# Kernel optimization log

Hardware: AMD Instinct MI355X
Metric: run time of the kernel (lower is better)

The kernel has to match this reference:

```python
import jax, jax.numpy as jnp
import numpy as np

B, N, G = 256, 512, 117  # batch, max_num_cells, n_genes
CH = 25                  # Emphsis conv out channels (hidden_d_1st_conv)


def setup_inputs() -> dict:
    key = jax.random.key(0)
    ks = jax.random.split(key, 11)
    images = jax.random.normal(ks[0], (B, N, 1, 7, 7), dtype=jnp.float32)
    spot_images = jax.random.normal(ks[1], (B, 1, 28, 28), dtype=jnp.float32)
    gene_expression = jax.random.normal(ks[2], (B, G), dtype=jnp.float32)
    # Emphsis: Conv2d(1, 25, k=3, s=1) + ReLU
    W_emph = jax.random.normal(ks[3], (CH, 1, 3, 3), dtype=jnp.float32) * 0.2
    b_emph = jax.random.normal(ks[4], (CH,), dtype=jnp.float32) * 0.1
    # 117 stacked GeneBlock Linear(625, 1) heads -> one (G, 625) matrix
    W_reg = jax.random.normal(ks[5], (G, 625), dtype=jnp.float32) * 0.04
    b_reg = jax.random.normal(ks[6], (G,), dtype=jnp.float32) * 0.1
    # PatchEmbedding: Conv2d(1, 3, k=5, s=5)
    W_patch = jax.random.normal(ks[7], (3, 1, 5, 5), dtype=jnp.float32) * 0.2
    b_patch = jax.random.normal(ks[8], (3,), dtype=jnp.float32) * 0.1
    # global_embedding: Linear(75, 1) + ELU
    W_glob = jax.random.normal(ks[9], (1, 75), dtype=jnp.float32) * 0.1
    b_glob = jax.random.normal(ks[10], (1,), dtype=jnp.float32) * 0.1
    return dict(images=images, spot_images=spot_images, gene_expression=gene_expression,
                W_emph=W_emph, b_emph=b_emph, W_reg=W_reg, b_reg=b_reg,
                W_patch=W_patch, b_patch=b_patch, W_glob=W_glob, b_glob=b_glob)


def reference(images, spot_images, gene_expression, W_emph, b_emph, W_reg, b_reg,
              W_patch, b_patch, W_glob, b_glob):
    Bn, Nc = images.shape[0], images.shape[1]
    # Emphsis conv over all (batch, cell) pairs at once: (B*N, 1, 7, 7) -> (B*N, 25, 5, 5)
    x = images.reshape(Bn * Nc, 1, 7, 7)
    t = jax.lax.conv_general_dilated(x, W_emph, window_strides=(1, 1), padding='VALID',
                                     dimension_numbers=('NCHW', 'OIHW', 'NCHW'))
    t = jax.nn.relu(t + b_emph[None, :, None, None])
    flat = t.reshape(Bn, Nc, CH * 5 * 5)  # (B, N, 625)
    # 117 independent Linear(625,1) heads fused into one matmul -> (B, N, G)
    out = jnp.einsum('bnd,gd->bng', flat, W_reg) + b_reg
    # PatchEmbedding: (B,1,28,28) -> (B,3,5,5) -> tokens (B,25,3) -> flatten (B,75)
    s = jax.lax.conv_general_dilated(spot_images, W_patch, window_strides=(5, 5), padding='VALID',
                                     dimension_numbers=('NCHW', 'OIHW', 'NCHW'))
    s = s + b_patch[None, :, None, None]
    s = s.reshape(Bn, 3, 25).transpose(0, 2, 1).reshape(Bn, 75)
    glob = jax.nn.elu(s @ W_glob.T + b_glob)  # (B, 1)
    # out1 broadcast of global embedding over (cells, genes)
    cell = jax.nn.relu(out + glob[:, :, None])  # (B, N, G)
    # F.linear with ones weight over cell axis == sum over cells
    spot = cell.sum(axis=1)  # (B, G)
    out1 = jnp.broadcast_to(glob[:, :, None], (Bn, Nc, out.shape[2]))  # (B, N, G)
    return spot, cell, out1
```

## Files before the change

### kernel.cpp

```cpp
#include <hip/hip_runtime.h>


typedef __attribute__((ext_vector_type(16))) float f32x16;
typedef __attribute__((ext_vector_type(8))) short short8;
typedef __attribute__((ext_vector_type(2))) unsigned int uint2v;
typedef __attribute__((ext_vector_type(4))) unsigned int uint4v;

#define WB_OFF    0
#define WBIG_OFF  163840
#define GLOB_OFF  245760
#define SPOT_OFF  246784

#define SPOT_OUT_OFF 0
#define CELL_OUT_OFF 29952
#define OUT1_OUT_OFF 15365376

__device__ __forceinline__ unsigned short f2bf(float x) {
  unsigned int u = __builtin_bit_cast(unsigned int, x);
  u = (u + 0x7FFFu + ((u >> 16) & 1u)) >> 16;
  return (unsigned short)u;
}

__device__ __forceinline__ unsigned int cvt_pk_bf16(float lo, float hi) {
  unsigned int w;
  asm("v_cvt_pk_bf16_f32 %0, %1, %2" : "=v"(w) : "v"(lo), "v"(hi));
  return w;
}

__global__ __launch_bounds__(128) void prep_kernel(
    const float* __restrict__ spot_images, const float* __restrict__ W_patch,
    const float* __restrict__ b_patch, const float* __restrict__ W_glob,
    const float* __restrict__ b_glob, const float* __restrict__ W_reg,
    const float* __restrict__ W_emph, const float* __restrict__ b_emph,
    unsigned short* __restrict__ wb, unsigned short* __restrict__ wbig,
    float* __restrict__ glob) {
  int bid = blockIdx.x;
  int tid = threadIdx.x;
  if (bid < 256) {
    __shared__ float red[75];
    if (tid < 75) {
      int token = tid / 3;
      int chan = tid - token * 3;
      int ty = token / 5, tx = token - ty * 5;
      const float* img = spot_images + bid * 784 + (ty * 5) * 28 + tx * 5;
      float a = 0.f;
      #pragma unroll
      for (int i = 0; i < 5; ++i)
        #pragma unroll
        for (int j = 0; j < 5; ++j)
          a = fmaf(img[i * 28 + j], W_patch[chan * 25 + i * 5 + j], a);
      a += b_patch[chan];
      red[tid] = a * W_glob[tid];
    }
    __syncthreads();
    if (tid == 0) {
      float s = b_glob[0];
      for (int k = 0; k < 75; ++k) s += red[k];
      glob[bid] = (s > 0.f) ? s : expm1f(s);
    }
  } else if (bid < 336) {
    int idx = bid - 256;
    int jt = idx >> 2, s = idx & 3;
    if (tid < 64) {
      int j = jt * 32 + (tid & 31);
      int h = tid >> 5;
      unsigned short hv[8];
      #pragma unroll
      for (int jj = 0; jj < 8; ++jj) {
        int i = s * 16 + h * 8 + jj;
        float val = 0.f;
        if (j < 625) {
          int ch = j / 25, p = j % 25;
          int oy = p / 5, ox = p - oy * 5;
          if (i < 49) {
            int iy = i / 7, ix = i - iy * 7;
            int ky = iy - oy, kx = ix - ox;
            if (ky >= 0 && ky < 3 && kx >= 0 && kx < 3)
              val = W_emph[ch * 9 + ky * 3 + kx];
          } else if (i == 49) {
            val = b_emph[ch];
          }
        }
        hv[jj] = f2bf(val);
      }
      unsigned int u[4];
      #pragma unroll
      for (int k = 0; k < 4; ++k)
        u[k] = (unsigned int)hv[2 * k] | ((unsigned int)hv[2 * k + 1] << 16);
      ((uint4*)wbig)[idx * 64 + tid] = make_uint4(u[0], u[1], u[2], u[3]);
    }
  } else {
    int idx = bid - 336;
    int sg = idx >> 2, wcp = idx & 3;
    if (tid < 64) {
      int g = wcp * 32 + (tid & 31);
      int h = tid >> 5;
      unsigned short hv[8];
      #pragma unroll
      for (int jj = 0; jj < 8; ++jj) {
        int k = sg * 16 + h * 8 + jj;
        float val = (g < 117 && k < 625) ? W_reg[g * 625 + k] : 0.f;
        hv[jj] = f2bf(val);
      }
      unsigned int u[4];
      #pragma unroll
      for (int k = 0; k < 4; ++k)
        u[k] = (unsigned int)hv[2 * k] | ((unsigned int)hv[2 * k + 1] << 16);
      ((uint4*)wb)[idx * 64 + tid] = make_uint4(u[0], u[1], u[2], u[3]);
    }
  }
}

__global__ __launch_bounds__(512, 4) void main_kernel(
    const float* __restrict__ images, const float* __restrict__ b_reg,
    const unsigned short* __restrict__ wb, const unsigned short* __restrict__ wbig,
    const float* __restrict__ glob, float* __restrict__ out,
    float* __restrict__ spotp) {
  __shared__ char smem[34816];
  unsigned short* imgbs = (unsigned short*)smem;
  float* C = (float*)smem;
  float* red = (float*)(smem + 32768);
  int tid = threadIdx.x;
  int bid = blockIdx.x;
  int b = bid >> 1, half = bid & 1;
  int n0 = half * 256;

  #pragma unroll
  for (int it = 0; it < 4; ++it) {
    int u = it * 512 + tid;
    int cell = u & 255, kc = u >> 8;
    const float* src = images + (size_t)(b * 512 + n0 + cell) * 49 + kc * 8;
    float v[8];
    #pragma unroll
    for (int j = 0; j < 8; ++j) v[j] = 0.f;
    if (kc < 6) {
      #pragma unroll
      for (int j = 0; j < 8; ++j) v[j] = src[j];
    } else if (kc == 6) {
      v[0] = src[0];
      v[1] = 1.0f;
    }
    unsigned int uu[4];
    #pragma unroll
    for (int k = 0; k < 4; ++k) uu[k] = cvt_pk_bf16(v[2 * k], v[2 * k + 1]);
    ((uint4*)imgbs)[kc * 256 + cell] = make_uint4(uu[0], uu[1], uu[2], uu[3]);
  }
  __syncthreads();

  int l = tid & 63;
  int ct = __builtin_amdgcn_readfirstlane(tid >> 6);
  int m = l & 31, hh = l >> 5;
  const short8* imgb8 = (const short8*)imgbs;
  const short8* wb8 = (const short8*)wb;
  const short8* wbig8 = (const short8*)wbig;

  short8 bi0 = imgb8[(0 + hh) * 256 + ct * 32 + m];
  short8 bi1 = imgb8[(2 + hh) * 256 + ct * 32 + m];
  short8 bi2 = imgb8[(4 + hh) * 256 + ct * 32 + m];
  short8 bi3 = imgb8[(6 + hh) * 256 + ct * 32 + m];

  f32x16 acc0, acc1, acc2, acc3;
  #pragma unroll
  for (int i = 0; i < 16; ++i) {
    acc0[i] = 0.f; acc1[i] = 0.f; acc2[i] = 0.f; acc3[i] = 0.f;
  }

  for (int jt = 0; jt < 20; ++jt) {
    int ab = jt * 256 + l;
    short8 a0 = wbig8[ab];
    short8 a1 = wbig8[ab + 64];
    short8 a2 = wbig8[ab + 128];
    short8 a3 = wbig8[ab + 192];

    f32x16 o;
    #pragma unroll
    for (int i = 0; i < 16; ++i) o[i] = 0.f;
    o = __builtin_amdgcn_mfma_f32_32x32x16_bf16(a0, bi0, o, 0, 0, 0);
    o = __builtin_amdgcn_mfma_f32_32x32x16_bf16(a1, bi1, o, 0, 0, 0);
    o = __builtin_amdgcn_mfma_f32_32x32x16_bf16(a2, bi2, o, 0, 0, 0);
    o = __builtin_amdgcn_mfma_f32_32x32x16_bf16(a3, bi3, o, 0, 0, 0);

    unsigned int W[8];
    #pragma unroll
    for (int q = 0; q < 8; ++q)
      W[q] = cvt_pk_bf16(fmaxf(o[2 * q], 0.f), fmaxf(o[2 * q + 1], 0.f));
    uint2v s02 = __builtin_amdgcn_permlane32_swap(W[0], W[2], false, false);
    uint2v s13 = __builtin_amdgcn_permlane32_swap(W[1], W[3], false, false);
    uint2v s46 = __builtin_amdgcn_permlane32_swap(W[4], W[6], false, false);
    uint2v s57 = __builtin_amdgcn_permlane32_swap(W[5], W[7], false, false);
    uint4v f0 = {s02[0], s13[0], s02[1], s13[1]};
    uint4v f1 = {s46[0], s57[0], s46[1], s57[1]};
    short8 af0 = __builtin_bit_cast(short8, f0);
    short8 af1 = __builtin_bit_cast(short8, f1);

    int kb = jt * 512 + l;
    acc0 = __builtin_amdgcn_mfma_f32_32x32x16_bf16(af0, wb8[kb], acc0, 0, 0, 0);
    acc1 = __builtin_amdgcn_mfma_f32_32x32x16_bf16(af0, wb8[kb + 64], acc1, 0, 0, 0);
    acc2 = __builtin_amdgcn_mfma_f32_32x32x16_bf16(af0, wb8[kb + 128], acc2, 0, 0, 0);
    acc3 = __builtin_amdgcn_mfma_f32_32x32x16_bf16(af0, wb8[kb + 192], acc3, 0, 0, 0);
    acc0 = __builtin_amdgcn_mfma_f32_32x32x16_bf16(af1, wb8[kb + 256], acc0, 0, 0, 0);
    acc1 = __builtin_amdgcn_mfma_f32_32x32x16_bf16(af1, wb8[kb + 320], acc1, 0, 0, 0);
    acc2 = __builtin_amdgcn_mfma_f32_32x32x16_bf16(af1, wb8[kb + 384], acc2, 0, 0, 0);
    acc3 = __builtin_amdgcn_mfma_f32_32x32x16_bf16(af1, wb8[kb + 448], acc3, 0, 0, 0);
  }
  __syncthreads();

  float gb = glob[b];
  float part = 0.f;
  size_t rowbase = (size_t)(b * 512 + n0);
  #pragma unroll
  for (int p = 0; p < 4; ++p) {
    if ((ct >> 1) == p) {
      int nb = (ct & 1) * 32;
      #define EPI(Q, ACC)                                                  \
        {                                                                  \
          int g = (Q)*32 + m;                                              \
          float br = (g < 117) ? b_reg[g] : 0.f;                           \
          _Pragma("unroll")                                                \
          for (int reg = 0; reg < 16; ++reg) {                             \
            int n = nb + (reg & 3) + 8 * (reg >> 2) + 4 * hh;              \
            C[n * 128 + g] = fmaxf(ACC[reg] + br + gb, 0.f);               \
          }                                                                \
        }
      EPI(0, acc0) EPI(1, acc1) EPI(2, acc2) EPI(3, acc3)
      #undef EPI
    }
    __syncthreads();
    float* cellchunk = out + CELL_OUT_OFF + (rowbase + p * 64) * 117;
    #pragma unroll
    for (int i = 0; i < 15; ++i) {
      int idx = i * 512 + tid;
      if (idx < 7488) {
        int n = idx / 117;
        int gg = idx - n * 117;
        cellchunk[idx] = C[n * 128 + gg];
      }
    }
    float4 gv = make_float4(gb, gb, gb, gb);
    float4* o1v = (float4*)(out + OUT1_OUT_OFF + (rowbase + p * 64) * 117);
    #pragma unroll
    for (int i = 0; i < 4; ++i) {
      int idx = i * 512 + tid;
      if (idx < 1872) o1v[idx] = gv;
    }
    {
      int grp = tid >> 7, t = tid & 127;
      float s = 0.f;
      #pragma unroll
      for (int n = 0; n < 16; ++n) s += C[(grp * 16 + n) * 128 + t];
      red[grp * 128 + t] = s;
    }
    __syncthreads();
    if (tid < 128)
      part += red[tid] + red[128 + tid] + red[256 + tid] + red[384 + tid];
  }
  if (tid < 128)
    spotp[(size_t)(b * 2 + half) * 128 + tid] = part;
}

__global__ __launch_bounds__(256) void spot_reduce(
    const float* __restrict__ spotp, float* __restrict__ out) {
  int idx = blockIdx.x * 256 + threadIdx.x;
  int b = idx / 117;
  int g = idx - b * 117;
  float s = spotp[(size_t)(b * 2 + 0) * 128 + g] +
            spotp[(size_t)(b * 2 + 1) * 128 + g];
  out[SPOT_OUT_OFF + idx] = s;
}

extern "C" void kernel_launch(void* const* d_in, const int* in_sizes, int n_in,
                              void* d_out, int out_size, void* d_ws, size_t ws_size,
                              hipStream_t stream) {
  const float* images      = (const float*)d_in[0];
  const float* spot_images = (const float*)d_in[1];
  const float* W_emph = (const float*)d_in[3];
  const float* b_emph = (const float*)d_in[4];
  const float* W_reg  = (const float*)d_in[5];
  const float* b_reg  = (const float*)d_in[6];
  const float* W_patch = (const float*)d_in[7];
  const float* b_patch = (const float*)d_in[8];
  const float* W_glob  = (const float*)d_in[9];
  const float* b_glob  = (const float*)d_in[10];
  float* out = (float*)d_out;

  unsigned short* wb   = (unsigned short*)((char*)d_ws + WB_OFF);
  unsigned short* wbig = (unsigned short*)((char*)d_ws + WBIG_OFF);
  float* glob  = (float*)((char*)d_ws + GLOB_OFF);
  float* spotp = (float*)((char*)d_ws + SPOT_OFF);

  prep_kernel<<<496, 128, 0, stream>>>(spot_images, W_patch, b_patch, W_glob,
                                       b_glob, W_reg, W_emph, b_emph, wb, wbig,
                                       glob);
  main_kernel<<<512, 512, 0, stream>>>(images, b_reg, wb, wbig, glob, out,
                                       spotp);
  spot_reduce<<<117, 256, 0, stream>>>(spotp, out);
}
```

Before: 61.87 us.

## Double-buffer combined weight tiles into LDS via async global_load_lds

Weights for both GEMM stages are interleaved per k-tile into one buffer. Each iteration asynchronously stages the next 12 KB tile into LDS with global_load_lds while computing on the current tile, replacing direct per-wave global loads. Because every wave read the same weights, they are now fetched once per block and shared, with the load latency meant to overlap compute. In exchange, LDS use per block rises to about 58 KB, which may limit occupancy, and a __syncthreads is added every iteration.

Measured after the change: 55.73 us. 1.11x faster.

```diff
diff --git a/kernel.cpp b/kernel.cpp
--- a/kernel.cpp
+++ b/kernel.cpp
@@ -6,8 +6,7 @@
 typedef __attribute__((ext_vector_type(2))) unsigned int uint2v;
 typedef __attribute__((ext_vector_type(4))) unsigned int uint4v;
 
-#define WB_OFF    0
-#define WBIG_OFF  163840
+#define WCOMB_OFF 0
 #define GLOB_OFF  245760
 #define SPOT_OFF  246784
 
@@ -25,6 +24,12 @@
   unsigned int w;
   asm("v_cvt_pk_bf16_f32 %0, %1, %2" : "=v"(w) : "v"(lo), "v"(hi));
   return w;
+}
+
+__device__ __forceinline__ void gload16(const void* g, void* l) {
+  __builtin_amdgcn_global_load_lds(
+      (const __attribute__((address_space(1))) void*)g,
+      (__attribute__((address_space(3))) void*)l, 16, 0, 0);
 }
 
 __global__ __launch_bounds__(128) void prep_kernel(
@@ -32,8 +37,7 @@
     const float* __restrict__ b_patch, const float* __restrict__ W_glob,
     const float* __restrict__ b_glob, const float* __restrict__ W_reg,
     const float* __restrict__ W_emph, const float* __restrict__ b_emph,
-    unsigned short* __restrict__ wb, unsigned short* __restrict__ wbig,
-    float* __restrict__ glob) {
+    unsigned short* __restrict__ wcomb, float* __restrict__ glob) {
   int bid = blockIdx.x;
   int tid = threadIdx.x;
   if (bid < 256) {
@@ -87,13 +91,13 @@
       #pragma unroll
       for (int k = 0; k < 4; ++k)
         u[k] = (unsigned int)hv[2 * k] | ((unsigned int)hv[2 * k + 1] << 16);
-      ((uint4*)wbig)[idx * 64 + tid] = make_uint4(u[0], u[1], u[2], u[3]);
+      ((uint4*)wcomb)[jt * 768 + s * 64 + tid] = make_uint4(u[0], u[1], u[2], u[3]);
     }
   } else {
     int idx = bid - 336;
-    int sg = idx >> 2, wcp = idx & 3;
+    int sg = idx >> 2, q = idx & 3;
     if (tid < 64) {
-      int g = wcp * 32 + (tid & 31);
+      int g = q * 32 + (tid & 31);
       int h = tid >> 5;
       unsigned short hv[8];
       #pragma unroll
@@ -106,24 +110,37 @@
       #pragma unroll
       for (int k = 0; k < 4; ++k)
         u[k] = (unsigned int)hv[2 * k] | ((unsigned int)hv[2 * k + 1] << 16);
-      ((uint4*)wb)[idx * 64 + tid] = make_uint4(u[0], u[1], u[2], u[3]);
+      int jt = sg >> 1, c = (sg & 1) * 4 + q;
+      ((uint4*)wcomb)[jt * 768 + 256 + c * 64 + tid] =
+          make_uint4(u[0], u[1], u[2], u[3]);
     }
   }
 }
 
 __global__ __launch_bounds__(512, 4) void main_kernel(
     const float* __restrict__ images, const float* __restrict__ b_reg,
-    const unsigned short* __restrict__ wb, const unsigned short* __restrict__ wbig,
-    const float* __restrict__ glob, float* __restrict__ out,
-    float* __restrict__ spotp) {
-  __shared__ char smem[34816];
+    const unsigned short* __restrict__ wcomb, const float* __restrict__ glob,
+    float* __restrict__ out, float* __restrict__ spotp) {
+  __shared__ char smem[59392];
   unsigned short* imgbs = (unsigned short*)smem;
+  char* wbuf = smem + 32768;
   float* C = (float*)smem;
-  float* red = (float*)(smem + 32768);
+  float* red = (float*)(smem + 57344);
   int tid = threadIdx.x;
   int bid = blockIdx.x;
   int b = bid >> 1, half = bid & 1;
   int n0 = half * 256;
+
+  int l = tid & 63;
+  int ct = __builtin_amdgcn_readfirstlane(tid >> 6);
+  const char* wcombB = (const char*)wcomb;
+
+  auto stage = [&](int jt, int buf) {
+    const char* s0 = wcombB + jt * 12288 + ct * 1024 + l * 16;
+    char* d0 = wbuf + buf * 12288 + ct * 1024;
+    gload16(s0, d0);
+    if (ct < 4) gload16(s0 + 8192, d0 + 8192);
+  };
 
   #pragma unroll
   for (int it = 0; it < 4; ++it) {
@@ -145,14 +162,11 @@
     for (int k = 0; k < 4; ++k) uu[k] = cvt_pk_bf16(v[2 * k], v[2 * k + 1]);
     ((uint4*)imgbs)[kc * 256 + cell] = make_uint4(uu[0], uu[1], uu[2], uu[3]);
   }
+  stage(0, 0);
   __syncthreads();
 
-  int l = tid & 63;
-  int ct = __builtin_amdgcn_readfirstlane(tid >> 6);
   int m = l & 31, hh = l >> 5;
   const short8* imgb8 = (const short8*)imgbs;
-  const short8* wb8 = (const short8*)wb;
-  const short8* wbig8 = (const short8*)wbig;
 
   short8 bi0 = imgb8[(0 + hh) * 256 + ct * 32 + m];
   short8 bi1 = imgb8[(2 + hh) * 256 + ct * 32 + m];
@@ -166,11 +180,13 @@
   }
 
   for (int jt = 0; jt < 20; ++jt) {
-    int ab = jt * 256 + l;
-    short8 a0 = wbig8[ab];
-    short8 a1 = wbig8[ab + 64];
-    short8 a2 = wbig8[ab + 128];
-    short8 a3 = wbig8[ab + 192];
+    if (jt < 19) stage(jt + 1, (jt + 1) & 1);
+
+    const short8* wB = (const short8*)(wbuf + (jt & 1) * 12288);
+    short8 a0 = wB[l];
+    short8 a1 = wB[64 + l];
+    short8 a2 = wB[128 + l];
+    short8 a3 = wB[192 + l];
 
     f32x16 o;
     #pragma unroll
@@ -193,17 +209,17 @@
     short8 af0 = __builtin_bit_cast(short8, f0);
     short8 af1 = __builtin_bit_cast(short8, f1);
 
-    int kb = jt * 512 + l;
-    acc0 = __builtin_amdgcn_mfma_f32_32x32x16_bf16(af0, wb8[kb], acc0, 0, 0, 0);
-    acc1 = __builtin_amdgcn_mfma_f32_32x32x16_bf16(af0, wb8[kb + 64], acc1, 0, 0, 0);
-    acc2 = __builtin_amdgcn_mfma_f32_32x32x16_bf16(af0, wb8[kb + 128], acc2, 0, 0, 0);
-    acc3 = __builtin_amdgcn_mfma_f32_32x32x16_bf16(af0, wb8[kb + 192], acc3, 0, 0, 0);
-    acc0 = __builtin_amdgcn_mfma_f32_32x32x16_bf16(af1, wb8[kb + 256], acc0, 0, 0, 0);
-    acc1 = __builtin_amdgcn_mfma_f32_32x32x16_bf16(af1, wb8[kb + 320], acc1, 0, 0, 0);
-    acc2 = __builtin_amdgcn_mfma_f32_32x32x16_bf16(af1, wb8[kb + 384], acc2, 0, 0, 0);
-    acc3 = __builtin_amdgcn_mfma_f32_32x32x16_bf16(af1, wb8[kb + 448], acc3, 0, 0, 0);
-  }
-  __syncthreads();
+    acc0 = __builtin_amdgcn_mfma_f32_32x32x16_bf16(af0, wB[256 + l], acc0, 0, 0, 0);
+    acc1 = __builtin_amdgcn_mfma_f32_32x32x16_bf16(af0, wB[320 + l], acc1, 0, 0, 0);
+    acc2 = __builtin_amdgcn_mfma_f32_32x32x16_bf16(af0, wB[384 + l], acc2, 0, 0, 0);
+    acc3 = __builtin_amdgcn_mfma_f32_32x32x16_bf16(af0, wB[448 + l], acc3, 0, 0, 0);
+    acc0 = __builtin_amdgcn_mfma_f32_32x32x16_bf16(af1, wB[512 + l], acc0, 0, 0, 0);
+    acc1 = __builtin_amdgcn_mfma_f32_32x32x16_bf16(af1, wB[576 + l], acc1, 0, 0, 0);
+    acc2 = __builtin_amdgcn_mfma_f32_32x32x16_bf16(af1, wB[640 + l], acc2, 0, 0, 0);
+    acc3 = __builtin_amdgcn_mfma_f32_32x32x16_bf16(af1, wB[704 + l], acc3, 0, 0, 0);
+
+    __syncthreads();
+  }
 
   float gb = glob[b];
   float part = 0.f;
@@ -283,15 +299,13 @@
   const float* b_glob  = (const float*)d_in[10];
   float* out = (float*)d_out;
 
-  unsigned short* wb   = (unsigned short*)((char*)d_ws + WB_OFF);
-  unsigned short* wbig = (unsigned short*)((char*)d_ws + WBIG_OFF);
+  unsigned short* wcomb = (unsigned short*)((char*)d_ws + WCOMB_OFF);
   float* glob  = (float*)((char*)d_ws + GLOB_OFF);
   float* spotp = (float*)((char*)d_ws + SPOT_OFF);
 
   prep_kernel<<<496, 128, 0, stream>>>(spot_images, W_patch, b_patch, W_glob,
-                                       b_glob, W_reg, W_emph, b_emph, wb, wbig,
+                                       b_glob, W_reg, W_emph, b_emph, wcomb,
                                        glob);
-  main_kernel<<<512, 512, 0, stream>>>(images, b_reg, wb, wbig, glob, out,
-                                       spotp);
+  main_kernel<<<512, 512, 0, stream>>>(images, b_reg, wcomb, glob, out, spotp);
   spot_reduce<<<117, 256, 0, stream>>>(spotp, out);
 }
```
